# Performance work log

Hardware: AMD Instinct MI355X
Metric: run time of the kernel (lower is better)

Reference implementation:

```python
import jax, jax.numpy as jnp
import numpy as np

MAX_LEVELS = 5
CHANNELS = 3


def _gauss_kernel(channels=CHANNELS):
    k = np.array([[1., 4., 6., 4., 1.],
                  [4., 16., 24., 16., 4.],
                  [6., 24., 36., 24., 6.],
                  [4., 16., 24., 16., 4.],
                  [1., 4., 6., 4., 1.]], dtype=np.float32) / 256.0
    return jnp.asarray(np.tile(k[None, None], (channels, 1, 1, 1)))  # (C,1,5,5)


def conv_gauss(img, kernel):
    # reflect-pad by 2 then depthwise 5x5 conv (groups = C)
    img = jnp.pad(img, ((0, 0), (0, 0), (2, 2), (2, 2)), mode='reflect')
    return jax.lax.conv_general_dilated(
        img, kernel, window_strides=(1, 1), padding='VALID',
        dimension_numbers=('NCHW', 'OIHW', 'NCHW'),
        feature_group_count=img.shape[1])


def downsample(x):
    return x[:, :, ::2, ::2]


def upsample(x, kernel):
    # zero-stuff: x at even (h,w) positions, zeros elsewhere, then smooth with 4*kernel
    b, c, h, w = x.shape
    up = jnp.zeros((b, c, 2 * h, 2 * w), dtype=x.dtype).at[:, :, ::2, ::2].set(x)
    return conv_gauss(up, 4.0 * kernel)


def laplacian_pyramid(img, kernel, max_levels=MAX_LEVELS):
    current = img
    pyr = []
    for _ in range(max_levels):
        filtered = conv_gauss(current, kernel)
        down = downsample(filtered)
        up = upsample(down, kernel)
        pyr.append(current - up)
        current = down
    return pyr


def setup_inputs() -> dict:
    key = jax.random.key(0)
    k1, k2 = jax.random.split(key)
    shape = (32, 3, 512, 512)
    return {
        'input': jax.random.normal(k1, shape, dtype=jnp.float32),
        'target': jax.random.normal(k2, shape, dtype=jnp.float32),
        'kernel': _gauss_kernel(CHANNELS),
    }


def reference(input, target, kernel):
    pyr_in = laplacian_pyramid(input, kernel, MAX_LEVELS)
    pyr_tg = laplacian_pyramid(target, kernel, MAX_LEVELS)
    # F.l1_loss default reduction: mean over all elements, per level
    return sum(jnp.mean(jnp.abs(a - b)) for a, b in zip(pyr_in, pyr_tg))
```

## Files before the change

### kernel.cpp

```cpp
#include <hip/hip_runtime.h>


#define BC 96
#define KA 0.0625f
#define KB 0.25f
#define KC 0.375f

__device__ __forceinline__ int refl(int i, int n) {
    if (i < 0) i = -i;
    if (i >= n) i = 2 * n - 2 - i;
    return i;
}

template<int H, int NC, bool DIFF>
__device__ __forceinline__ void load_row(const float* __restrict__ pa,
                                         const float* __restrict__ pb,
                                         int r, int basec, float* __restrict__ c) {
    const int off = r * H + basec;
    if constexpr (NC == 8) {
        float4 a0 = *(const float4*)(pa + off);
        float4 a1 = *(const float4*)(pa + off + 4);
        c[0]=a0.x; c[1]=a0.y; c[2]=a0.z; c[3]=a0.w;
        c[4]=a1.x; c[5]=a1.y; c[6]=a1.z; c[7]=a1.w;
        if constexpr (DIFF) {
            float4 b0 = *(const float4*)(pb + off);
            float4 b1 = *(const float4*)(pb + off + 4);
            c[0]-=b0.x; c[1]-=b0.y; c[2]-=b0.z; c[3]-=b0.w;
            c[4]-=b1.x; c[5]-=b1.y; c[6]-=b1.z; c[7]-=b1.w;
        }
    } else if constexpr (NC == 4) {
        float4 a0 = *(const float4*)(pa + off);
        c[0]=a0.x; c[1]=a0.y; c[2]=a0.z; c[3]=a0.w;
        if constexpr (DIFF) {
            float4 b0 = *(const float4*)(pb + off);
            c[0]-=b0.x; c[1]-=b0.y; c[2]-=b0.z; c[3]-=b0.w;
        }
    } else {
        float2 a0 = *(const float2*)(pa + off);
        c[0]=a0.x; c[1]=a0.y;
        if constexpr (DIFF) {
            float2 b0 = *(const float2*)(pb + off);
            c[0]-=b0.x; c[1]-=b0.y;
        }
    }
}

template<int NC>
__device__ __forceinline__ void hconv(const float* __restrict__ c,
                                      float* __restrict__ o, int lane) {
    constexpr int ND = NC / 2;
    float e[NC + 3];
#pragma unroll
    for (int i = 0; i < NC; ++i) e[i + 2] = c[i];
    const bool l0 = (lane == 0), l63 = (lane == 63);
    { float v = __shfl(e[NC + 1], lane - 1); e[1] = l0 ? e[3] : v; }
    if constexpr (NC >= 4) {
        { float v = __shfl(e[NC], lane - 1); e[0] = l0 ? e[4] : v; }
        { float v = __shfl(e[2], lane + 1); e[NC + 2] = l63 ? e[NC] : v; }
    } else {
        e[0] = __shfl(e[2], l0 ? 1 : lane - 1);
        e[NC + 2] = __shfl(e[2], l63 ? 63 : lane + 1);
    }
#pragma unroll
    for (int j = 0; j < ND; ++j)
        o[j] = KA * e[2*j] + KB * e[2*j+1] + KC * e[2*j+2]
             + KB * e[2*j+3] + KA * e[2*j+4];
}

template<int H, int NC, bool DIFF, int R>
__global__ __launch_bounds__(256) void lap_slide(
        const float* __restrict__ A, const float* __restrict__ B,
        float* __restrict__ down, float* __restrict__ out, float invN) {
    constexpr int Hd = H / 2, ND = NC / 2, SPP = H / R;
    __shared__ float red[4];
    const int tid = threadIdx.x;
    const int lane = tid & 63, wid = tid >> 6;
    const int sid = blockIdx.x * 4 + wid;
    const int bc = sid / SPP;
    const int y0 = (sid % SPP) * R;
    const float* pa = A + (size_t)bc * H * H;
    const float* pb = DIFF ? (B + (size_t)bc * H * H) : nullptr;
    float* pd = down + (size_t)bc * Hd * Hd;
    const int basec = lane * NC;

    float h0[ND], h1[ND], h2[ND], h3[ND], h4[ND];
    float w0[NC], w1[NC], w2[NC];
#pragma unroll
    for (int i = 0; i < NC; ++i) { w0[i] = 0.f; w1[i] = 0.f; w2[i] = 0.f; }
    float acc = 0.f;
    float c[NC];

    const int d0 = y0 >> 1;
    int dbeg = d0 - 1; if (dbeg < 0) dbeg = 0;
    const int dend = d0 + R / 2;

    load_row<H,NC,DIFF>(pa, pb, refl(2*dbeg - 2, H), basec, c); hconv<NC>(c, h0, lane);
    load_row<H,NC,DIFF>(pa, pb, refl(2*dbeg - 1, H), basec, c); hconv<NC>(c, h1, lane);
    load_row<H,NC,DIFF>(pa, pb, refl(2*dbeg,     H), basec, c); hconv<NC>(c, h2, lane);

    for (int d = dbeg; d <= dend; ++d) {
        load_row<H,NC,DIFF>(pa, pb, refl(2*d + 1, H), basec, c); hconv<NC>(c, h3, lane);
        load_row<H,NC,DIFF>(pa, pb, refl(2*d + 2, H), basec, c); hconv<NC>(c, h4, lane);

        float dn[ND];
#pragma unroll
        for (int j = 0; j < ND; ++j)
            dn[j] = KA*h0[j] + KB*h1[j] + KC*h2[j] + KB*h3[j] + KA*h4[j];

        if (d >= d0 && d < d0 + R/2) {
            const int doff = d * Hd + lane * ND;
            if constexpr (ND == 4) {
                float4 s; s.x = dn[0]; s.y = dn[1]; s.z = dn[2]; s.w = dn[3];
                *(float4*)(pd + doff) = s;
            } else if constexpr (ND == 2) {
                float2 s; s.x = dn[0]; s.y = dn[1];
                *(float2*)(pd + doff) = s;
            } else {
                pd[doff] = dn[0];
            }
        }

        float dm, dp;
        if constexpr (ND >= 2) {
            { float v = __shfl(dn[ND-1], lane - 1); dm = (lane == 0)  ? dn[1]    : v; }
            { float v = __shfl(dn[0],    lane + 1); dp = (lane == 63) ? dn[ND-1] : v; }
        } else {
            dm = __shfl(dn[0], (lane == 0)  ? 1  : lane - 1);
            dp = __shfl(dn[0], (lane == 63) ? 63 : lane + 1);
        }
#pragma unroll
        for (int i = 0; i < NC; ++i) { w0[i] = w1[i]; w1[i] = w2[i]; }
#pragma unroll
        for (int j = 0; j < ND; ++j) {
            float lf = j ? dn[j-1] : dm;
            float rg = (j + 1 < ND) ? dn[j+1] : dp;
            w2[2*j]     = 0.125f * lf + 0.75f * dn[j] + 0.125f * rg;
            w2[2*j + 1] = 0.5f * (dn[j] + rg);
        }

        if (d >= d0 + 1) {
            const int ye = 2 * d - 2;
            float ce[NC], co[NC];
            load_row<H,NC,DIFF>(pa, pb, ye,     basec, ce);
            load_row<H,NC,DIFF>(pa, pb, ye + 1, basec, co);
            if (ye == 0) {
#pragma unroll
                for (int i = 0; i < NC; ++i) {
                    acc += fabsf(ce[i] - (0.75f*w1[i] + 0.25f*w2[i]));
                    acc += fabsf(co[i] - 0.5f*(w1[i] + w2[i]));
                }
            } else if (ye == H - 2) {
#pragma unroll
                for (int i = 0; i < NC; ++i) {
                    acc += fabsf(ce[i] - (0.125f*w0[i] + 0.875f*w1[i]));
                    acc += fabsf(co[i] - w1[i]);
                }
            } else {
#pragma unroll
                for (int i = 0; i < NC; ++i) {
                    acc += fabsf(ce[i] - (0.125f*w0[i] + 0.75f*w1[i] + 0.125f*w2[i]));
                    acc += fabsf(co[i] - 0.5f*(w1[i] + w2[i]));
                }
            }
        }
#pragma unroll
        for (int j = 0; j < ND; ++j) { h0[j] = h2[j]; h1[j] = h3[j]; h2[j] = h4[j]; }
    }

#pragma unroll
    for (int off2 = 32; off2 > 0; off2 >>= 1)
        acc += __shfl_down(acc, off2, 64);
    if (lane == 0) red[wid] = acc;
    __syncthreads();
    if (tid == 0)
        atomicAdd(out, (red[0] + red[1] + red[2] + red[3]) * invN);
}

__global__ __launch_bounds__(256) void lap_small(
        const float* __restrict__ dsrc, float* __restrict__ out,
        float invN3, float invN4) {
    __shared__ float p[64 * 66];
    __shared__ float hh[64 * 34];
    __shared__ float dd[32 * 34];
    __shared__ float W3[32 * 64];
    __shared__ float h4[32 * 18];
    __shared__ float d4[16 * 18];
    __shared__ float W4[16 * 32];
    __shared__ float red[4];
    const int tid = threadIdx.x;
    const float* src = dsrc + (size_t)blockIdx.x * 4096;
    for (int i = tid; i < 4096; i += 256)
        p[(i >> 6) * 66 + (i & 63)] = src[i];
    __syncthreads();
    const float k[5] = {KA, KB, KC, KB, KA};
    for (int i = tid; i < 64 * 32; i += 256) {
        int r = i >> 5, t = i & 31;
        const float* pr = p + r * 66;
        float s = 0.f;
#pragma unroll
        for (int v = 0; v < 5; ++v) s += k[v] * pr[refl(2*t + v - 2, 64)];
        hh[r * 34 + t] = s;
    }
    __syncthreads();
    for (int i = tid; i < 32 * 32; i += 256) {
        int dy = i >> 5, t = i & 31;
        float s = 0.f;
#pragma unroll
        for (int u = 0; u < 5; ++u) s += k[u] * hh[refl(2*dy + u - 2, 64) * 34 + t];
        dd[dy * 34 + t] = s;
    }
    __syncthreads();
    for (int i = tid; i < 32 * 32; i += 256) {
        int a = i >> 5, t = i & 31;
        const float* dr = dd + a * 34;
        float dm = dr[t == 0 ? 1 : t - 1];
        float dc = dr[t];
        float dp = dr[t == 31 ? 31 : t + 1];
        W3[a * 64 + 2*t]     = 0.125f * dm + 0.75f * dc + 0.125f * dp;
        W3[a * 64 + 2*t + 1] = 0.5f * (dc + dp);
    }
    __syncthreads();
    float acc3 = 0.f;
    for (int i = tid; i < 4096; i += 256) {
        int y = i >> 6, x = i & 63;
        float cur = p[y * 66 + x];
        float up;
        if ((y & 1) == 0) {
            int a0 = refl(y - 2, 64) >> 1, a1 = y >> 1, a2 = refl(y + 2, 64) >> 1;
            up = 0.125f*W3[a0*64 + x] + 0.75f*W3[a1*64 + x] + 0.125f*W3[a2*64 + x];
        } else {
            int a0 = (y - 1) >> 1, a1 = refl(y + 1, 64) >> 1;
            up = 0.5f * (W3[a0*64 + x] + W3[a1*64 + x]);
        }
        acc3 += fabsf(cur - up);
    }
    __syncthreads();
    for (int i = tid; i < 32 * 16; i += 256) {
        int r = i >> 4, t = i & 15;
        const float* pr = dd + r * 34;
        float s = 0.f;
#pragma unroll
        for (int v = 0; v < 5; ++v) s += k[v] * pr[refl(2*t + v - 2, 32)];
        h4[r * 18 + t] = s;
    }
    __syncthreads();
    for (int i = tid; i < 16 * 16; i += 256) {
        int dy = i >> 4, t = i & 15;
        float s = 0.f;
#pragma unroll
        for (int u = 0; u < 5; ++u) s += k[u] * h4[refl(2*dy + u - 2, 32) * 18 + t];
        d4[dy * 18 + t] = s;
    }
    __syncthreads();
    for (int i = tid; i < 16 * 16; i += 256) {
        int a = i >> 4, t = i & 15;
        const float* dr = d4 + a * 18;
        float dm = dr[t == 0 ? 1 : t - 1];
        float dc = dr[t];
        float dp = dr[t == 15 ? 15 : t + 1];
        W4[a * 32 + 2*t]     = 0.125f * dm + 0.75f * dc + 0.125f * dp;
        W4[a * 32 + 2*t + 1] = 0.5f * (dc + dp);
    }
    __syncthreads();
    float acc4 = 0.f;
    for (int i = tid; i < 1024; i += 256) {
        int y = i >> 5, x = i & 31;
        float cur = dd[y * 34 + x];
        float up;
        if ((y & 1) == 0) {
            int a0 = refl(y - 2, 32) >> 1, a1 = y >> 1, a2 = refl(y + 2, 32) >> 1;
            up = 0.125f*W4[a0*32 + x] + 0.75f*W4[a1*32 + x] + 0.125f*W4[a2*32 + x];
        } else {
            int a0 = (y - 1) >> 1, a1 = refl(y + 1, 32) >> 1;
            up = 0.5f * (W4[a0*32 + x] + W4[a1*32 + x]);
        }
        acc4 += fabsf(cur - up);
    }
    float acc = acc3 * invN3 + acc4 * invN4;
#pragma unroll
    for (int off2 = 32; off2 > 0; off2 >>= 1)
        acc += __shfl_down(acc, off2, 64);
    int lane = tid & 63, wid = tid >> 6;
    if (lane == 0) red[wid] = acc;
    __syncthreads();
    if (tid == 0)
        atomicAdd(out, red[0] + red[1] + red[2] + red[3]);
}

extern "C" void kernel_launch(void* const* d_in, const int* in_sizes, int n_in,
                              void* d_out, int out_size, void* d_ws, size_t ws_size,
                              hipStream_t stream) {
    const float* in = (const float*)d_in[0];
    const float* tg = (const float*)d_in[1];
    float* out = (float*)d_out;
    float* ws = (float*)d_ws;

    float* down0 = ws;
    float* down1 = down0 + (size_t)BC * 256 * 256;
    float* down2 = down1 + (size_t)BC * 128 * 128;

    hipMemsetAsync(out, 0, sizeof(float), stream);

    lap_slide<512, 8, true, 16><<<96 * 32 / 4, 256, 0, stream>>>(
        in, tg, down0, out, 1.f / (96.f * 512.f * 512.f));
    lap_slide<256, 4, false, 16><<<96 * 16 / 4, 256, 0, stream>>>(
        down0, nullptr, down1, out, 1.f / (96.f * 256.f * 256.f));
    lap_slide<128, 2, false, 16><<<96 * 8 / 4, 256, 0, stream>>>(
        down1, nullptr, down2, out, 1.f / (96.f * 128.f * 128.f));
    lap_small<<<BC, 256, 0, stream>>>(
        down2, out, 1.f / (96.f * 64.f * 64.f), 1.f / (96.f * 32.f * 32.f));
}
```

Baseline: 273.1 us.

## Prefetch rows in registers, reuse loaded rows for residual, raise small-level parallelism

The sliding-window kernel now issues the global loads for the next two rows one iteration ahead and keeps the raw values in registers. The residual pass reuses rows already loaded for the blur (eMid/oPrev history) instead of reloading both input tensors. Levels 1 and 2 use shorter strips with more blocks, and the small-level kernel runs with 1024 threads per block. These changes target load latency, redundant global traffic and low occupancy on the later levels, at the cost of higher register pressure and more halo recomputation per strip.

```diff
diff --git a/kernel.cpp b/kernel.cpp
--- a/kernel.cpp
+++ b/kernel.cpp
@@ -13,36 +13,46 @@
 }
 
 template<int H, int NC, bool DIFF>
-__device__ __forceinline__ void load_row(const float* __restrict__ pa,
+__device__ __forceinline__ void load_raw(const float* __restrict__ pa,
                                          const float* __restrict__ pb,
-                                         int r, int basec, float* __restrict__ c) {
+                                         int r, int basec,
+                                         float* __restrict__ a,
+                                         float* __restrict__ b) {
     const int off = r * H + basec;
     if constexpr (NC == 8) {
         float4 a0 = *(const float4*)(pa + off);
         float4 a1 = *(const float4*)(pa + off + 4);
-        c[0]=a0.x; c[1]=a0.y; c[2]=a0.z; c[3]=a0.w;
-        c[4]=a1.x; c[5]=a1.y; c[6]=a1.z; c[7]=a1.w;
+        a[0]=a0.x; a[1]=a0.y; a[2]=a0.z; a[3]=a0.w;
+        a[4]=a1.x; a[5]=a1.y; a[6]=a1.z; a[7]=a1.w;
         if constexpr (DIFF) {
             float4 b0 = *(const float4*)(pb + off);
             float4 b1 = *(const float4*)(pb + off + 4);
-            c[0]-=b0.x; c[1]-=b0.y; c[2]-=b0.z; c[3]-=b0.w;
-            c[4]-=b1.x; c[5]-=b1.y; c[6]-=b1.z; c[7]-=b1.w;
+            b[0]=b0.x; b[1]=b0.y; b[2]=b0.z; b[3]=b0.w;
+            b[4]=b1.x; b[5]=b1.y; b[6]=b1.z; b[7]=b1.w;
         }
     } else if constexpr (NC == 4) {
         float4 a0 = *(const float4*)(pa + off);
-        c[0]=a0.x; c[1]=a0.y; c[2]=a0.z; c[3]=a0.w;
+        a[0]=a0.x; a[1]=a0.y; a[2]=a0.z; a[3]=a0.w;
         if constexpr (DIFF) {
             float4 b0 = *(const float4*)(pb + off);
-            c[0]-=b0.x; c[1]-=b0.y; c[2]-=b0.z; c[3]-=b0.w;
+            b[0]=b0.x; b[1]=b0.y; b[2]=b0.z; b[3]=b0.w;
         }
     } else {
         float2 a0 = *(const float2*)(pa + off);
-        c[0]=a0.x; c[1]=a0.y;
+        a[0]=a0.x; a[1]=a0.y;
         if constexpr (DIFF) {
             float2 b0 = *(const float2*)(pb + off);
-            c[0]-=b0.x; c[1]-=b0.y;
-        }
-    }
+            b[0]=b0.x; b[1]=b0.y;
+        }
+    }
+}
+
+template<int NC, bool DIFF>
+__device__ __forceinline__ void materialize(const float* __restrict__ a,
+                                            const float* __restrict__ b,
+                                            float* __restrict__ c) {
+#pragma unroll
+    for (int i = 0; i < NC; ++i) c[i] = DIFF ? (a[i] - b[i]) : a[i];
 }
 
 template<int NC>
@@ -85,22 +95,37 @@
 
     float h0[ND], h1[ND], h2[ND], h3[ND], h4[ND];
     float w0[NC], w1[NC], w2[NC];
-#pragma unroll
-    for (int i = 0; i < NC; ++i) { w0[i] = 0.f; w1[i] = 0.f; w2[i] = 0.f; }
+    float eOld[NC], eMid[NC], oPrev[NC];
+    float nA1[NC], nB1[NC], nA2[NC], nB2[NC];
+    float c1[NC], c2[NC], t[NC], tb[NC];
+#pragma unroll
+    for (int i = 0; i < NC; ++i) {
+        w0[i] = 0.f; w1[i] = 0.f; w2[i] = 0.f;
+        eOld[i] = 0.f; oPrev[i] = 0.f;
+    }
     float acc = 0.f;
-    float c[NC];
 
     const int d0 = y0 >> 1;
     int dbeg = d0 - 1; if (dbeg < 0) dbeg = 0;
     const int dend = d0 + R / 2;
 
-    load_row<H,NC,DIFF>(pa, pb, refl(2*dbeg - 2, H), basec, c); hconv<NC>(c, h0, lane);
-    load_row<H,NC,DIFF>(pa, pb, refl(2*dbeg - 1, H), basec, c); hconv<NC>(c, h1, lane);
-    load_row<H,NC,DIFF>(pa, pb, refl(2*dbeg,     H), basec, c); hconv<NC>(c, h2, lane);
+    load_raw<H,NC,DIFF>(pa, pb, refl(2*dbeg - 2, H), basec, t, tb);
+    materialize<NC,DIFF>(t, tb, c1); hconv<NC>(c1, h0, lane);
+    load_raw<H,NC,DIFF>(pa, pb, refl(2*dbeg - 1, H), basec, t, tb);
+    materialize<NC,DIFF>(t, tb, c1); hconv<NC>(c1, h1, lane);
+    load_raw<H,NC,DIFF>(pa, pb, refl(2*dbeg, H), basec, t, tb);
+    materialize<NC,DIFF>(t, tb, eMid); hconv<NC>(eMid, h2, lane);
+    load_raw<H,NC,DIFF>(pa, pb, refl(2*dbeg + 1, H), basec, nA1, nB1);
+    load_raw<H,NC,DIFF>(pa, pb, refl(2*dbeg + 2, H), basec, nA2, nB2);
 
     for (int d = dbeg; d <= dend; ++d) {
-        load_row<H,NC,DIFF>(pa, pb, refl(2*d + 1, H), basec, c); hconv<NC>(c, h3, lane);
-        load_row<H,NC,DIFF>(pa, pb, refl(2*d + 2, H), basec, c); hconv<NC>(c, h4, lane);
+        materialize<NC,DIFF>(nA1, nB1, c1);
+        materialize<NC,DIFF>(nA2, nB2, c2);
+        load_raw<H,NC,DIFF>(pa, pb, refl(2*d + 3, H), basec, nA1, nB1);
+        load_raw<H,NC,DIFF>(pa, pb, refl(2*d + 4, H), basec, nA2, nB2);
+
+        hconv<NC>(c1, h3, lane);
+        hconv<NC>(c2, h4, lane);
 
         float dn[ND];
 #pragma unroll
@@ -110,10 +135,10 @@
         if (d >= d0 && d < d0 + R/2) {
             const int doff = d * Hd + lane * ND;
             if constexpr (ND == 4) {
-                float4 s; s.x = dn[0]; s.y = dn[1]; s.z = dn[2]; s.w = dn[3];
+                float4 s; s.x=dn[0]; s.y=dn[1]; s.z=dn[2]; s.w=dn[3];
                 *(float4*)(pd + doff) = s;
             } else if constexpr (ND == 2) {
-                float2 s; s.x = dn[0]; s.y = dn[1];
+                float2 s; s.x=dn[0]; s.y=dn[1];
                 *(float2*)(pd + doff) = s;
             } else {
                 pd[doff] = dn[0];
@@ -140,28 +165,30 @@
 
         if (d >= d0 + 1) {
             const int ye = 2 * d - 2;
-            float ce[NC], co[NC];
-            load_row<H,NC,DIFF>(pa, pb, ye,     basec, ce);
-            load_row<H,NC,DIFF>(pa, pb, ye + 1, basec, co);
             if (ye == 0) {
 #pragma unroll
                 for (int i = 0; i < NC; ++i) {
-                    acc += fabsf(ce[i] - (0.75f*w1[i] + 0.25f*w2[i]));
-                    acc += fabsf(co[i] - 0.5f*(w1[i] + w2[i]));
+                    acc += fabsf(eOld[i]  - (0.75f*w1[i] + 0.25f*w2[i]));
+                    acc += fabsf(oPrev[i] - 0.5f*(w1[i] + w2[i]));
                 }
             } else if (ye == H - 2) {
 #pragma unroll
                 for (int i = 0; i < NC; ++i) {
-                    acc += fabsf(ce[i] - (0.125f*w0[i] + 0.875f*w1[i]));
-                    acc += fabsf(co[i] - w1[i]);
+                    acc += fabsf(eOld[i]  - (0.125f*w0[i] + 0.875f*w1[i]));
+                    acc += fabsf(oPrev[i] - w1[i]);
                 }
             } else {
 #pragma unroll
                 for (int i = 0; i < NC; ++i) {
-                    acc += fabsf(ce[i] - (0.125f*w0[i] + 0.75f*w1[i] + 0.125f*w2[i]));
-                    acc += fabsf(co[i] - 0.5f*(w1[i] + w2[i]));
+                    acc += fabsf(eOld[i]  - (0.125f*w0[i] + 0.75f*w1[i] + 0.125f*w2[i]));
+                    acc += fabsf(oPrev[i] - 0.5f*(w1[i] + w2[i]));
                 }
             }
+        }
+
+#pragma unroll
+        for (int i = 0; i < NC; ++i) {
+            eOld[i] = eMid[i]; eMid[i] = c2[i]; oPrev[i] = c1[i];
         }
 #pragma unroll
         for (int j = 0; j < ND; ++j) { h0[j] = h2[j]; h1[j] = h3[j]; h2[j] = h4[j]; }
@@ -176,7 +203,7 @@
         atomicAdd(out, (red[0] + red[1] + red[2] + red[3]) * invN);
 }
 
-__global__ __launch_bounds__(256) void lap_small(
+__global__ __launch_bounds__(1024) void lap_small(
         const float* __restrict__ dsrc, float* __restrict__ out,
         float invN3, float invN4) {
     __shared__ float p[64 * 66];
@@ -186,14 +213,14 @@
     __shared__ float h4[32 * 18];
     __shared__ float d4[16 * 18];
     __shared__ float W4[16 * 32];
-    __shared__ float red[4];
+    __shared__ float red[16];
     const int tid = threadIdx.x;
     const float* src = dsrc + (size_t)blockIdx.x * 4096;
-    for (int i = tid; i < 4096; i += 256)
+    for (int i = tid; i < 4096; i += 1024)
         p[(i >> 6) * 66 + (i & 63)] = src[i];
     __syncthreads();
     const float k[5] = {KA, KB, KC, KB, KA};
-    for (int i = tid; i < 64 * 32; i += 256) {
+    for (int i = tid; i < 64 * 32; i += 1024) {
         int r = i >> 5, t = i & 31;
         const float* pr = p + r * 66;
         float s = 0.f;
@@ -202,7 +229,7 @@
         hh[r * 34 + t] = s;
     }
     __syncthreads();
-    for (int i = tid; i < 32 * 32; i += 256) {
+    for (int i = tid; i < 32 * 32; i += 1024) {
         int dy = i >> 5, t = i & 31;
         float s = 0.f;
 #pragma unroll
@@ -210,7 +237,7 @@
         dd[dy * 34 + t] = s;
     }
     __syncthreads();
-    for (int i = tid; i < 32 * 32; i += 256) {
+    for (int i = tid; i < 32 * 32; i += 1024) {
         int a = i >> 5, t = i & 31;
         const float* dr = dd + a * 34;
         float dm = dr[t == 0 ? 1 : t - 1];
@@ -221,7 +248,7 @@
     }
     __syncthreads();
     float acc3 = 0.f;
-    for (int i = tid; i < 4096; i += 256) {
+    for (int i = tid; i < 4096; i += 1024) {
         int y = i >> 6, x = i & 63;
         float cur = p[y * 66 + x];
         float up;
@@ -235,7 +262,7 @@
         acc3 += fabsf(cur - up);
     }
     __syncthreads();
-    for (int i = tid; i < 32 * 16; i += 256) {
+    for (int i = tid; i < 32 * 16; i += 1024) {
         int r = i >> 4, t = i & 15;
         const float* pr = dd + r * 34;
         float s = 0.f;
@@ -244,7 +271,7 @@
         h4[r * 18 + t] = s;
     }
     __syncthreads();
-    for (int i = tid; i < 16 * 16; i += 256) {
+    for (int i = tid; i < 16 * 16; i += 1024) {
         int dy = i >> 4, t = i & 15;
         float s = 0.f;
 #pragma unroll
@@ -252,7 +279,7 @@
         d4[dy * 18 + t] = s;
     }
     __syncthreads();
-    for (int i = tid; i < 16 * 16; i += 256) {
+    for (int i = tid; i < 16 * 16; i += 1024) {
         int a = i >> 4, t = i & 15;
         const float* dr = d4 + a * 18;
         float dm = dr[t == 0 ? 1 : t - 1];
@@ -263,7 +290,7 @@
     }
     __syncthreads();
     float acc4 = 0.f;
-    for (int i = tid; i < 1024; i += 256) {
+    for (int i = tid; i < 1024; i += 1024) {
         int y = i >> 5, x = i & 31;
         float cur = dd[y * 34 + x];
         float up;
@@ -283,8 +310,12 @@
     int lane = tid & 63, wid = tid >> 6;
     if (lane == 0) red[wid] = acc;
     __syncthreads();
-    if (tid == 0)
-        atomicAdd(out, red[0] + red[1] + red[2] + red[3]);
+    if (tid == 0) {
+        float s = 0.f;
+#pragma unroll
+        for (int i = 0; i < 16; ++i) s += red[i];
+        atomicAdd(out, s);
+    }
 }
 
 extern "C" void kernel_launch(void* const* d_in, const int* in_sizes, int n_in,
@@ -303,10 +334,10 @@
 
     lap_slide<512, 8, true, 16><<<96 * 32 / 4, 256, 0, stream>>>(
         in, tg, down0, out, 1.f / (96.f * 512.f * 512.f));
-    lap_slide<256, 4, false, 16><<<96 * 16 / 4, 256, 0, stream>>>(
+    lap_slide<256, 4, false, 8><<<96 * 32 / 4, 256, 0, stream>>>(
         down0, nullptr, down1, out, 1.f / (96.f * 256.f * 256.f));
-    lap_slide<128, 2, false, 16><<<96 * 8 / 4, 256, 0, stream>>>(
+    lap_slide<128, 2, false, 4><<<96 * 32 / 4, 256, 0, stream>>>(
         down1, nullptr, down2, out, 1.f / (96.f * 128.f * 128.f));
-    lap_small<<<BC, 256, 0, stream>>>(
+    lap_small<<<BC, 1024, 0, stream>>>(
         down2, out, 1.f / (96.f * 64.f * 64.f), 1.f / (96.f * 32.f * 32.f));
 }
```

Result: faster. 261.4 us (-4.3%).
